# Kernel tuning notes

Measured on AMD Instinct MI355X. Metric: run time of the kernel, lower is better.

The kernel has to match this reference:

```python
import jax, jax.numpy as jnp
import numpy as np


def _lstm_gates(z, c):
    # Keras LSTMCell gate order: i, f, c(candidate), o
    i, f, g, o = jnp.split(z, 4, axis=-1)
    c_new = jax.nn.sigmoid(f) * c + jax.nn.sigmoid(i) * jnp.tanh(g)
    h_new = jax.nn.sigmoid(o) * jnp.tanh(c_new)
    return h_new, c_new


def setup_inputs() -> dict:
    key = jax.random.key(0)
    ks = jax.random.split(key, 12)
    BS, T, F, Z, H = 8192, 20, 80, 32, 256
    s = 0.05
    return {
        "x": jax.random.normal(ks[0], (BS, T, F), jnp.float32),
        "z1": jax.random.normal(ks[1], (BS, Z), jnp.float32),
        "z2": jax.random.normal(ks[2], (BS, Z), jnp.float32),
        "eps": jax.random.normal(ks[3], (BS, T, F), jnp.float32),
        "W1": jax.random.normal(ks[4], (2 * Z, 4 * H), jnp.float32) * s,
        "U1": jax.random.normal(ks[5], (H, 4 * H), jnp.float32) * s,
        "b1": jnp.zeros((4 * H,), jnp.float32),
        "W2": jax.random.normal(ks[6], (H, 4 * H), jnp.float32) * s,
        "U2": jax.random.normal(ks[7], (H, 4 * H), jnp.float32) * s,
        "b2": jnp.zeros((4 * H,), jnp.float32),
        "Wmu": jax.random.normal(ks[8], (H, F), jnp.float32) * s,
        "bmu": jnp.zeros((F,), jnp.float32),
        "Wlv": jax.random.normal(ks[9], (H, F), jnp.float32) * s,
        "blv": jnp.zeros((F,), jnp.float32),
    }


def reference(x, z1, z2, eps, W1, U1, b1, W2, U2, b2, Wmu, bmu, Wlv, blv):
    bs, T = x.shape[0], x.shape[1]
    H = U1.shape[0]
    # z1,z2 are tiled across time -> per-step RNN input is constant, so the
    # input projection of layer 1 can be hoisted out of the scan.
    z_cat = jnp.concatenate([z1, z2], axis=-1)          # [bs, 2Z]
    xw1 = z_cat @ W1 + b1                                # [bs, 4H] constant per step

    def step(carry, _):
        h1, c1, h2, c2 = carry
        h1n, c1n = _lstm_gates(xw1 + h1 @ U1, c1)
        h2n, c2n = _lstm_gates(h1n @ W2 + b2 + h2 @ U2, c2)
        return (h1n, c1n, h2n, c2n), h2n

    zero = jnp.zeros((bs, H), x.dtype)
    _, hs = jax.lax.scan(step, (zero, zero, zero, zero), None, length=T)
    output = jnp.transpose(hs, (1, 0, 2))                # [bs, T, H]

    x_mu = output @ Wmu + bmu                            # [bs, T, F]
    x_logvar = output @ Wlv + blv                        # [bs, T, F]
    # NOTE: original code calls reparameterize(x_logvar_t, x_mu_t) with
    # swapped arguments -> sample = eps * exp(0.5 * x_mu) + x_logvar
    x_sample = eps * jnp.exp(0.5 * x_mu) + x_logvar
    return output, x_mu, x_logvar, x_sample
```

## Files before the change

### kernel.cpp

```cpp
#include <hip/hip_runtime.h>
#include <cstdint>
#include <cstddef>

typedef __bf16 bf16_t;
typedef __attribute__((ext_vector_type(8))) __bf16 bf16x8;
typedef __attribute__((ext_vector_type(4))) __bf16 bf16x4;
typedef __attribute__((ext_vector_type(4))) float f32x4;

#define TSTEPS 20
#define HDIM 256
#define GDIM 1024

static __device__ __forceinline__ f32x4 mfma_(bf16x8 a, bf16x8 b, f32x4 c) {
    return __builtin_amdgcn_mfma_f32_16x16x32_bf16(a, b, c, 0, 0, 0);
}
static __device__ __forceinline__ float sig_(float x) {
    return __builtin_amdgcn_rcpf(1.0f + __expf(-x));
}
static __device__ __forceinline__ float tanh_(float x) {
    return 2.0f * __builtin_amdgcn_rcpf(1.0f + __expf(-2.0f * x)) - 1.0f;
}

__global__ void pack_b_kernel(const float* __restrict__ srcA, int ldA,
                              const float* __restrict__ srcB, int ldB,
                              int split, int ntiles, int ktiles,
                              bf16_t* __restrict__ dst)
{
    int tid = blockIdx.x * blockDim.x + threadIdx.x;
    int total = ntiles * ktiles * 64;
    if (tid >= total) return;
    int lane = tid & 63;
    int tile = tid >> 6;
    int kt = tile % ktiles;
    int nt = tile / ktiles;
    int c  = (nt << 4) + (lane & 15);
    int k0 = (kt << 5) + ((lane >> 4) << 3);
    bf16x8 v;
    #pragma unroll
    for (int e = 0; e < 8; ++e) {
        int k = k0 + e;
        float x;
        if (c < split) x = srcA[(size_t)k * ldA + c];
        else           x = srcB[(size_t)k * ldB + (c - split)];
        v[e] = (bf16_t)x;
    }
    *reinterpret_cast<bf16x8*>(&dst[(size_t)tid * 8]) = v;
}

__global__ __launch_bounds__(256, 1)
void lstm_scan_kernel(const float* __restrict__ z1, const float* __restrict__ z2,
                      const float* __restrict__ W1, const float* __restrict__ b1,
                      const float* __restrict__ b2,
                      const bf16_t* __restrict__ U1p, const bf16_t* __restrict__ B2p,
                      float* __restrict__ out)
{
    __shared__ alignas(16) bf16_t xw1T[GDIM * 32];
    __shared__ alignas(16) bf16_t h1buf[2 * 32 * HDIM];
    __shared__ alignas(16) bf16_t h2buf[2 * 32 * HDIM];
    __shared__ alignas(16) float  zT[64 * 32];

    const int tid  = threadIdx.x;
    const int lane = tid & 63;
    const int wv   = tid >> 6;
    const int l15  = lane & 15;
    const int lq   = lane >> 4;
    const int w4   = wv << 2;
    const int b0   = blockIdx.x << 5;

    for (int i = tid; i < 2048; i += 256) {
        int r = i >> 6, k = i & 63;
        float v = (k < 32) ? z1[(size_t)(b0 + r) * 32 + k]
                           : z2[(size_t)(b0 + r) * 32 + (k - 32)];
        zT[k * 32 + r] = v;
    }
    for (int i = tid; i < 8192; i += 256) {
        h1buf[i] = (bf16_t)0.0f;
        h2buf[i] = (bf16_t)0.0f;
    }
    __syncthreads();

    for (int cc = 0; cc < 4; ++cc) {
        const int c = tid + (cc << 8);
        float acc[32];
        #pragma unroll
        for (int r = 0; r < 32; ++r) acc[r] = 0.0f;
        for (int k = 0; k < 64; ++k) {
            float wk = W1[k * GDIM + c];
            const f32x4* zp = reinterpret_cast<const f32x4*>(&zT[k * 32]);
            #pragma unroll
            for (int rq = 0; rq < 8; ++rq) {
                f32x4 z4 = zp[rq];
                #pragma unroll
                for (int j = 0; j < 4; ++j) acc[rq * 4 + j] += z4[j] * wk;
            }
        }
        const float bb = b1[c];
        const int sw = (c & 7) << 2;
        #pragma unroll
        for (int r = 0; r < 32; ++r)
            xw1T[((c << 5) + r) ^ sw] = (bf16_t)(acc[r] + bb);
    }

    float b2r[4][4];
    #pragma unroll
    for (int g = 0; g < 4; ++g)
        #pragma unroll
        for (int ht = 0; ht < 4; ++ht)
            b2r[g][ht] = b2[(((g << 4) + w4 + ht) << 4) + l15];

    f32x4 c1[2][4], c2[2][4];
    #pragma unroll
    for (int mt = 0; mt < 2; ++mt)
        #pragma unroll
        for (int ht = 0; ht < 4; ++ht) {
            c1[mt][ht] = (f32x4){0.f, 0.f, 0.f, 0.f};
            c2[mt][ht] = (f32x4){0.f, 0.f, 0.f, 0.f};
        }

    __syncthreads();

    bf16x8 af[2][16];
    const size_t outbase = (size_t)b0 * (TSTEPS * HDIM);

    for (int t = 0; t < TSTEPS; ++t) {
        const int cur = (t & 1) << 13;
        const int nxt = 8192 - cur;

        #pragma unroll
        for (int mt = 0; mt < 2; ++mt)
            #pragma unroll
            for (int kt = 0; kt < 8; ++kt) {
                int row = (mt << 4) + l15;
                int k0  = (kt << 5) + (lq << 3);
                int off = (((row << 8) + k0)) ^ ((row & 7) << 3);
                af[mt][kt] = *reinterpret_cast<const bf16x8*>(&h1buf[cur + off]);
            }

        #pragma unroll
        for (int ht = 0; ht < 4; ++ht) {
            f32x4 ag[2][4];
            #pragma unroll
            for (int g = 0; g < 4; ++g) {
                const int ntg  = (g << 4) + w4 + ht;
                const int colb = (ntg << 4) + l15;
                {
                    const int sw = (colb & 7) << 2;
                    int idx0 = ((colb << 5) + (lq << 2)) ^ sw;
                    int idx1 = ((colb << 5) + 16 + (lq << 2)) ^ sw;
                    bf16x4 v0 = *reinterpret_cast<const bf16x4*>(&xw1T[idx0]);
                    bf16x4 v1 = *reinterpret_cast<const bf16x4*>(&xw1T[idx1]);
                    f32x4 a0, a1;
                    #pragma unroll
                    for (int j = 0; j < 4; ++j) { a0[j] = (float)v0[j]; a1[j] = (float)v1[j]; }
                    ag[0][g] = a0; ag[1][g] = a1;
                }
                const bf16x8* bp = reinterpret_cast<const bf16x8*>(U1p) + ((ntg << 3) << 6) + lane;
                #pragma unroll
                for (int kt = 0; kt < 8; ++kt) {
                    bf16x8 bfr = bp[kt << 6];
                    ag[0][g] = mfma_(af[0][kt], bfr, ag[0][g]);
                    ag[1][g] = mfma_(af[1][kt], bfr, ag[1][g]);
                }
            }
            const int col = ((w4 + ht) << 4) + l15;
            #pragma unroll
            for (int mt = 0; mt < 2; ++mt)
                #pragma unroll
                for (int j = 0; j < 4; ++j) {
                    float iv = sig_(ag[mt][0][j]);
                    float fv = sig_(ag[mt][1][j]);
                    float gv = tanh_(ag[mt][2][j]);
                    float ov = sig_(ag[mt][3][j]);
                    float cn = fv * c1[mt][ht][j] + iv * gv;
                    c1[mt][ht][j] = cn;
                    float hn = ov * tanh_(cn);
                    int row = (mt << 4) + (lq << 2) + j;
                    h1buf[nxt + (((row << 8) + col) ^ ((row & 7) << 3))] = (bf16_t)hn;
                }
        }
        __syncthreads();

        #pragma unroll
        for (int mt = 0; mt < 2; ++mt)
            #pragma unroll
            for (int kt = 0; kt < 8; ++kt) {
                int row = (mt << 4) + l15;
                int k0  = (kt << 5) + (lq << 3);
                int off = (((row << 8) + k0)) ^ ((row & 7) << 3);
                af[mt][kt]     = *reinterpret_cast<const bf16x8*>(&h1buf[nxt + off]);
                af[mt][8 + kt] = *reinterpret_cast<const bf16x8*>(&h2buf[cur + off]);
            }

        #pragma unroll
        for (int ht = 0; ht < 4; ++ht) {
            f32x4 ag[2][4];
            #pragma unroll
            for (int g = 0; g < 4; ++g) {
                const int ntg = (g << 4) + w4 + ht;
                const float bb = b2r[g][ht];
                ag[0][g] = (f32x4){bb, bb, bb, bb};
                ag[1][g] = (f32x4){bb, bb, bb, bb};
                const bf16x8* bp0 = reinterpret_cast<const bf16x8*>(B2p) + ((ntg << 3) << 6) + lane;
                const bf16x8* bp1 = reinterpret_cast<const bf16x8*>(B2p) + (((64 + ntg) << 3) << 6) + lane;
                #pragma unroll
                for (int kt = 0; kt < 8; ++kt) {
                    bf16x8 bfr = bp0[kt << 6];
                    ag[0][g] = mfma_(af[0][kt], bfr, ag[0][g]);
                    ag[1][g] = mfma_(af[1][kt], bfr, ag[1][g]);
                }
                #pragma unroll
                for (int kt = 0; kt < 8; ++kt) {
                    bf16x8 bfr = bp1[kt << 6];
                    ag[0][g] = mfma_(af[0][8 + kt], bfr, ag[0][g]);
                    ag[1][g] = mfma_(af[1][8 + kt], bfr, ag[1][g]);
                }
            }
            const int col = ((w4 + ht) << 4) + l15;
            #pragma unroll
            for (int mt = 0; mt < 2; ++mt)
                #pragma unroll
                for (int j = 0; j < 4; ++j) {
                    float iv = sig_(ag[mt][0][j]);
                    float fv = sig_(ag[mt][1][j]);
                    float gv = tanh_(ag[mt][2][j]);
                    float ov = sig_(ag[mt][3][j]);
                    float cn = fv * c2[mt][ht][j] + iv * gv;
                    c2[mt][ht][j] = cn;
                    float hn = ov * tanh_(cn);
                    int row = (mt << 4) + (lq << 2) + j;
                    h2buf[nxt + (((row << 8) + col) ^ ((row & 7) << 3))] = (bf16_t)hn;
                    out[outbase + (size_t)row * (TSTEPS * HDIM) + t * HDIM + col] = hn;
                }
        }
        __syncthreads();
    }
}

__global__ __launch_bounds__(256, 1)
void proj_kernel(const float* __restrict__ outp, const float* __restrict__ eps,
                 const float* __restrict__ bmu, const float* __restrict__ blv,
                 const bf16_t* __restrict__ Wpp,
                 float* __restrict__ xmu, float* __restrict__ xlv, float* __restrict__ xsm)
{
    const int tid = threadIdx.x, lane = tid & 63, wv = tid >> 6;
    const int l15 = lane & 15, lq = lane >> 4;
    const size_t r0 = (size_t)blockIdx.x * 128 + (size_t)wv * 32;

    bf16x8 af[2][8];
    #pragma unroll
    for (int mt = 0; mt < 2; ++mt)
        #pragma unroll
        for (int kt = 0; kt < 8; ++kt) {
            const float* p = &outp[(r0 + (mt << 4) + l15) * 256 + (kt << 5) + (lq << 3)];
            f32x4 x0 = *reinterpret_cast<const f32x4*>(p);
            f32x4 x1 = *reinterpret_cast<const f32x4*>(p + 4);
            bf16x8 a;
            #pragma unroll
            for (int j = 0; j < 4; ++j) { a[j] = (bf16_t)x0[j]; a[4 + j] = (bf16_t)x1[j]; }
            af[mt][kt] = a;
        }

    f32x4 acc[2][10];
    #pragma unroll
    for (int mt = 0; mt < 2; ++mt)
        #pragma unroll
        for (int nt = 0; nt < 10; ++nt) acc[mt][nt] = (f32x4){0.f, 0.f, 0.f, 0.f};

    #pragma unroll
    for (int nt = 0; nt < 10; ++nt) {
        const bf16x8* bp = reinterpret_cast<const bf16x8*>(Wpp) + ((nt << 3) << 6) + lane;
        #pragma unroll
        for (int kt = 0; kt < 8; ++kt) {
            bf16x8 b = bp[kt << 6];
            acc[0][nt] = mfma_(af[0][kt], b, acc[0][nt]);
            acc[1][nt] = mfma_(af[1][kt], b, acc[1][nt]);
        }
    }

    #pragma unroll
    for (int mt = 0; mt < 2; ++mt)
        #pragma unroll
        for (int nt = 0; nt < 5; ++nt) {
            const int col = (nt << 4) + l15;
            const float bm = bmu[col], bl = blv[col];
            #pragma unroll
            for (int j = 0; j < 4; ++j) {
                size_t row = r0 + (mt << 4) + (lq << 2) + j;
                float mu = acc[mt][nt][j] + bm;
                float lv = acc[mt][5 + nt][j] + bl;
                size_t o = row * 80 + col;
                float sm = eps[o] * __expf(0.5f * mu) + lv;
                xmu[o] = mu; xlv[o] = lv; xsm[o] = sm;
            }
        }
}

extern "C" void kernel_launch(void* const* d_in, const int* in_sizes, int n_in,
                              void* d_out, int out_size, void* d_ws, size_t ws_size,
                              hipStream_t stream) {
    const float* z1  = (const float*)d_in[1];
    const float* z2  = (const float*)d_in[2];
    const float* eps = (const float*)d_in[3];
    const float* W1  = (const float*)d_in[4];
    const float* U1  = (const float*)d_in[5];
    const float* b1  = (const float*)d_in[6];
    const float* W2  = (const float*)d_in[7];
    const float* U2  = (const float*)d_in[8];
    const float* b2  = (const float*)d_in[9];
    const float* Wmu = (const float*)d_in[10];
    const float* bmu = (const float*)d_in[11];
    const float* Wlv = (const float*)d_in[12];
    const float* blv = (const float*)d_in[13];

    float* out0 = (float*)d_out;
    const size_t N_OUT = (size_t)8192 * 20 * 256;
    const size_t N_F   = (size_t)8192 * 20 * 80;
    float* xmu = out0 + N_OUT;
    float* xlv = xmu + N_F;
    float* xsm = xlv + N_F;

    bf16_t* U1p = (bf16_t*)d_ws;
    bf16_t* B2p = U1p + 262144;
    bf16_t* Wpp = U1p + 786432;

    pack_b_kernel<<<128, 256, 0, stream>>>(U1, 1024, U1, 1024, 1 << 30, 64, 8, U1p);
    pack_b_kernel<<<128, 256, 0, stream>>>(W2, 1024, W2, 1024, 1 << 30, 64, 8, B2p);
    pack_b_kernel<<<128, 256, 0, stream>>>(U2, 1024, U2, 1024, 1 << 30, 64, 8, B2p + 262144);
    pack_b_kernel<<<20, 256, 0, stream>>>(Wmu, 80, Wlv, 80, 80, 10, 8, Wpp);

    lstm_scan_kernel<<<256, 256, 0, stream>>>(z1, z2, W1, b1, b2, U1p, B2p, out0);
    proj_kernel<<<1280, 256, 0, stream>>>(out0, eps, bmu, blv, Wpp, xmu, xlv, xsm);
}
```

Measured before the change: 2.741 ms.

## Recompute layer-1 input projection via MFMA, double scan waves, restage proj via LDS

The scan kernel now runs 512 threads per block, with each wave owning two hidden tiles instead of four. It drops the scalar fp32 precompute of the z@W1 projection held in LDS and recomputes that projection with MFMA every step from packed bf16 W1, which frees LDS and registers. The projection kernel stages 64 rows through a swizzled LDS buffer before its MFMA, and outputs are written with nontemporal stores. This trades extra per-step MFMA work and a W1 pack for better occupancy and latency hiding in the serial scan.

```diff
diff --git a/kernel.cpp b/kernel.cpp
--- a/kernel.cpp
+++ b/kernel.cpp
@@ -8,8 +8,6 @@
 typedef __attribute__((ext_vector_type(4))) float f32x4;
 
 #define TSTEPS 20
-#define HDIM 256
-#define GDIM 1024
 
 static __device__ __forceinline__ f32x4 mfma_(bf16x8 a, bf16x8 b, f32x4 c) {
     return __builtin_amdgcn_mfma_f32_16x16x32_bf16(a, b, c, 0, 0, 0);
@@ -19,6 +17,9 @@
 }
 static __device__ __forceinline__ float tanh_(float x) {
     return 2.0f * __builtin_amdgcn_rcpf(1.0f + __expf(-2.0f * x)) - 1.0f;
+}
+static __device__ __forceinline__ int swz(int row, int k) {
+    return ((row << 8) + k) ^ ((row & 7) << 3);
 }
 
 __global__ void pack_b_kernel(const float* __restrict__ srcA, int ldA,
@@ -47,252 +48,272 @@
     *reinterpret_cast<bf16x8*>(&dst[(size_t)tid * 8]) = v;
 }
 
-__global__ __launch_bounds__(256, 1)
+__global__ __launch_bounds__(512, 2)
 void lstm_scan_kernel(const float* __restrict__ z1, const float* __restrict__ z2,
-                      const float* __restrict__ W1, const float* __restrict__ b1,
-                      const float* __restrict__ b2,
-                      const bf16_t* __restrict__ U1p, const bf16_t* __restrict__ B2p,
+                      const float* __restrict__ b1, const float* __restrict__ b2,
+                      const bf16x8* __restrict__ W1f, const bf16x8* __restrict__ U1f,
+                      const bf16x8* __restrict__ B2f,
                       float* __restrict__ out)
 {
-    __shared__ alignas(16) bf16_t xw1T[GDIM * 32];
-    __shared__ alignas(16) bf16_t h1buf[2 * 32 * HDIM];
-    __shared__ alignas(16) bf16_t h2buf[2 * 32 * HDIM];
-    __shared__ alignas(16) float  zT[64 * 32];
+    __shared__ alignas(16) bf16_t h1buf[2 * 32 * 256];
+    __shared__ alignas(16) bf16_t h2buf[2 * 32 * 256];
+    __shared__ alignas(16) bf16_t zc[32 * 64];
 
     const int tid  = threadIdx.x;
     const int lane = tid & 63;
     const int wv   = tid >> 6;
     const int l15  = lane & 15;
     const int lq   = lane >> 4;
-    const int w4   = wv << 2;
     const int b0   = blockIdx.x << 5;
 
-    for (int i = tid; i < 2048; i += 256) {
+    {
+        bf16x8 z8;
+        #pragma unroll
+        for (int j = 0; j < 8; ++j) z8[j] = (bf16_t)0.0f;
+        bf16x8* h1v = reinterpret_cast<bf16x8*>(h1buf);
+        bf16x8* h2v = reinterpret_cast<bf16x8*>(h2buf);
+        for (int i = tid; i < 2048; i += 512) { h1v[i] = z8; h2v[i] = z8; }
+    }
+    for (int i = tid; i < 2048; i += 512) {
         int r = i >> 6, k = i & 63;
         float v = (k < 32) ? z1[(size_t)(b0 + r) * 32 + k]
                            : z2[(size_t)(b0 + r) * 32 + (k - 32)];
-        zT[k * 32 + r] = v;
-    }
-    for (int i = tid; i < 8192; i += 256) {
-        h1buf[i] = (bf16_t)0.0f;
-        h2buf[i] = (bf16_t)0.0f;
+        zc[i] = (bf16_t)v;
     }
     __syncthreads();
 
-    for (int cc = 0; cc < 4; ++cc) {
-        const int c = tid + (cc << 8);
-        float acc[32];
-        #pragma unroll
-        for (int r = 0; r < 32; ++r) acc[r] = 0.0f;
-        for (int k = 0; k < 64; ++k) {
-            float wk = W1[k * GDIM + c];
-            const f32x4* zp = reinterpret_cast<const f32x4*>(&zT[k * 32]);
-            #pragma unroll
-            for (int rq = 0; rq < 8; ++rq) {
-                f32x4 z4 = zp[rq];
-                #pragma unroll
-                for (int j = 0; j < 4; ++j) acc[rq * 4 + j] += z4[j] * wk;
-            }
-        }
-        const float bb = b1[c];
-        const int sw = (c & 7) << 2;
-        #pragma unroll
-        for (int r = 0; r < 32; ++r)
-            xw1T[((c << 5) + r) ^ sw] = (bf16_t)(acc[r] + bb);
-    }
-
-    float b2r[4][4];
-    #pragma unroll
-    for (int g = 0; g < 4; ++g)
-        #pragma unroll
-        for (int ht = 0; ht < 4; ++ht)
-            b2r[g][ht] = b2[(((g << 4) + w4 + ht) << 4) + l15];
-
-    f32x4 c1[2][4], c2[2][4];
+    bf16x8 zf[2][2];
     #pragma unroll
     for (int mt = 0; mt < 2; ++mt)
         #pragma unroll
-        for (int ht = 0; ht < 4; ++ht) {
+        for (int kt = 0; kt < 2; ++kt)
+            zf[mt][kt] = *reinterpret_cast<const bf16x8*>(
+                &zc[((mt << 4) + l15) * 64 + (kt << 5) + (lq << 3)]);
+
+    float b1r[2][4], b2r[2][4];
+    #pragma unroll
+    for (int ht = 0; ht < 2; ++ht)
+        #pragma unroll
+        for (int g = 0; g < 4; ++g) {
+            const int ntg = (g << 4) + (wv << 1) + ht;
+            b1r[ht][g] = b1[(ntg << 4) + l15];
+            b2r[ht][g] = b2[(ntg << 4) + l15];
+        }
+
+    f32x4 c1[2][2], c2[2][2];
+    #pragma unroll
+    for (int mt = 0; mt < 2; ++mt)
+        #pragma unroll
+        for (int ht = 0; ht < 2; ++ht) {
             c1[mt][ht] = (f32x4){0.f, 0.f, 0.f, 0.f};
             c2[mt][ht] = (f32x4){0.f, 0.f, 0.f, 0.f};
         }
 
-    __syncthreads();
-
-    bf16x8 af[2][16];
-    const size_t outbase = (size_t)b0 * (TSTEPS * HDIM);
+    const size_t outbase = (size_t)b0 * (TSTEPS * 256);
 
     for (int t = 0; t < TSTEPS; ++t) {
         const int cur = (t & 1) << 13;
         const int nxt = 8192 - cur;
 
-        #pragma unroll
-        for (int mt = 0; mt < 2; ++mt)
-            #pragma unroll
-            for (int kt = 0; kt < 8; ++kt) {
-                int row = (mt << 4) + l15;
-                int k0  = (kt << 5) + (lq << 3);
-                int off = (((row << 8) + k0)) ^ ((row & 7) << 3);
-                af[mt][kt] = *reinterpret_cast<const bf16x8*>(&h1buf[cur + off]);
+        f32x4 ag[2][2][4];
+        #pragma unroll
+        for (int ht = 0; ht < 2; ++ht)
+            #pragma unroll
+            for (int g = 0; g < 4; ++g) {
+                const float b = b1r[ht][g];
+                ag[ht][0][g] = (f32x4){b, b, b, b};
+                ag[ht][1][g] = (f32x4){b, b, b, b};
             }
 
-        #pragma unroll
-        for (int ht = 0; ht < 4; ++ht) {
-            f32x4 ag[2][4];
-            #pragma unroll
-            for (int g = 0; g < 4; ++g) {
-                const int ntg  = (g << 4) + w4 + ht;
-                const int colb = (ntg << 4) + l15;
-                {
-                    const int sw = (colb & 7) << 2;
-                    int idx0 = ((colb << 5) + (lq << 2)) ^ sw;
-                    int idx1 = ((colb << 5) + 16 + (lq << 2)) ^ sw;
-                    bf16x4 v0 = *reinterpret_cast<const bf16x4*>(&xw1T[idx0]);
-                    bf16x4 v1 = *reinterpret_cast<const bf16x4*>(&xw1T[idx1]);
-                    f32x4 a0, a1;
+        {
+            bf16x8 af[2][8];
+            #pragma unroll
+            for (int mt = 0; mt < 2; ++mt)
+                #pragma unroll
+                for (int kt = 0; kt < 8; ++kt) {
+                    int row = (mt << 4) + l15;
+                    af[mt][kt] = *reinterpret_cast<const bf16x8*>(
+                        &h1buf[cur + swz(row, (kt << 5) + (lq << 3))]);
+                }
+            #pragma unroll
+            for (int ht = 0; ht < 2; ++ht)
+                #pragma unroll
+                for (int g = 0; g < 4; ++g) {
+                    const int ntg = (g << 4) + (wv << 1) + ht;
+                    const bf16x8* wz = W1f + ((ntg << 1) << 6) + lane;
                     #pragma unroll
-                    for (int j = 0; j < 4; ++j) { a0[j] = (float)v0[j]; a1[j] = (float)v1[j]; }
-                    ag[0][g] = a0; ag[1][g] = a1;
-                }
-                const bf16x8* bp = reinterpret_cast<const bf16x8*>(U1p) + ((ntg << 3) << 6) + lane;
-                #pragma unroll
-                for (int kt = 0; kt < 8; ++kt) {
-                    bf16x8 bfr = bp[kt << 6];
-                    ag[0][g] = mfma_(af[0][kt], bfr, ag[0][g]);
-                    ag[1][g] = mfma_(af[1][kt], bfr, ag[1][g]);
-                }
-            }
-            const int col = ((w4 + ht) << 4) + l15;
+                    for (int kt = 0; kt < 2; ++kt) {
+                        bf16x8 w = wz[kt << 6];
+                        ag[ht][0][g] = mfma_(zf[0][kt], w, ag[ht][0][g]);
+                        ag[ht][1][g] = mfma_(zf[1][kt], w, ag[ht][1][g]);
+                    }
+                    const bf16x8* wu = U1f + ((ntg << 3) << 6) + lane;
+                    #pragma unroll
+                    for (int kt = 0; kt < 8; ++kt) {
+                        bf16x8 w = wu[kt << 6];
+                        ag[ht][0][g] = mfma_(af[0][kt], w, ag[ht][0][g]);
+                        ag[ht][1][g] = mfma_(af[1][kt], w, ag[ht][1][g]);
+                    }
+                }
+        }
+        #pragma unroll
+        for (int ht = 0; ht < 2; ++ht) {
+            const int colb = (((wv << 1) + ht) << 4) + l15;
             #pragma unroll
             for (int mt = 0; mt < 2; ++mt)
                 #pragma unroll
                 for (int j = 0; j < 4; ++j) {
-                    float iv = sig_(ag[mt][0][j]);
-                    float fv = sig_(ag[mt][1][j]);
-                    float gv = tanh_(ag[mt][2][j]);
-                    float ov = sig_(ag[mt][3][j]);
+                    float iv = sig_(ag[ht][mt][0][j]);
+                    float fv = sig_(ag[ht][mt][1][j]);
+                    float gv = tanh_(ag[ht][mt][2][j]);
+                    float ov = sig_(ag[ht][mt][3][j]);
                     float cn = fv * c1[mt][ht][j] + iv * gv;
                     c1[mt][ht][j] = cn;
                     float hn = ov * tanh_(cn);
                     int row = (mt << 4) + (lq << 2) + j;
-                    h1buf[nxt + (((row << 8) + col) ^ ((row & 7) << 3))] = (bf16_t)hn;
+                    h1buf[nxt + swz(row, colb)] = (bf16_t)hn;
                 }
         }
         __syncthreads();
 
         #pragma unroll
-        for (int mt = 0; mt < 2; ++mt)
-            #pragma unroll
-            for (int kt = 0; kt < 8; ++kt) {
-                int row = (mt << 4) + l15;
-                int k0  = (kt << 5) + (lq << 3);
-                int off = (((row << 8) + k0)) ^ ((row & 7) << 3);
-                af[mt][kt]     = *reinterpret_cast<const bf16x8*>(&h1buf[nxt + off]);
-                af[mt][8 + kt] = *reinterpret_cast<const bf16x8*>(&h2buf[cur + off]);
+        for (int ht = 0; ht < 2; ++ht)
+            #pragma unroll
+            for (int g = 0; g < 4; ++g) {
+                const float b = b2r[ht][g];
+                ag[ht][0][g] = (f32x4){b, b, b, b};
+                ag[ht][1][g] = (f32x4){b, b, b, b};
             }
-
-        #pragma unroll
-        for (int ht = 0; ht < 4; ++ht) {
-            f32x4 ag[2][4];
-            #pragma unroll
-            for (int g = 0; g < 4; ++g) {
-                const int ntg = (g << 4) + w4 + ht;
-                const float bb = b2r[g][ht];
-                ag[0][g] = (f32x4){bb, bb, bb, bb};
-                ag[1][g] = (f32x4){bb, bb, bb, bb};
-                const bf16x8* bp0 = reinterpret_cast<const bf16x8*>(B2p) + ((ntg << 3) << 6) + lane;
-                const bf16x8* bp1 = reinterpret_cast<const bf16x8*>(B2p) + (((64 + ntg) << 3) << 6) + lane;
+        {
+            bf16x8 af[2][8];
+            #pragma unroll
+            for (int mt = 0; mt < 2; ++mt)
                 #pragma unroll
                 for (int kt = 0; kt < 8; ++kt) {
-                    bf16x8 bfr = bp0[kt << 6];
-                    ag[0][g] = mfma_(af[0][kt], bfr, ag[0][g]);
-                    ag[1][g] = mfma_(af[1][kt], bfr, ag[1][g]);
-                }
+                    int row = (mt << 4) + l15;
+                    af[mt][kt] = *reinterpret_cast<const bf16x8*>(
+                        &h1buf[nxt + swz(row, (kt << 5) + (lq << 3))]);
+                }
+            #pragma unroll
+            for (int ht = 0; ht < 2; ++ht)
+                #pragma unroll
+                for (int g = 0; g < 4; ++g) {
+                    const int ntg = (g << 4) + (wv << 1) + ht;
+                    const bf16x8* w2 = B2f + ((ntg << 3) << 6) + lane;
+                    #pragma unroll
+                    for (int kt = 0; kt < 8; ++kt) {
+                        bf16x8 w = w2[kt << 6];
+                        ag[ht][0][g] = mfma_(af[0][kt], w, ag[ht][0][g]);
+                        ag[ht][1][g] = mfma_(af[1][kt], w, ag[ht][1][g]);
+                    }
+                }
+            #pragma unroll
+            for (int mt = 0; mt < 2; ++mt)
                 #pragma unroll
                 for (int kt = 0; kt < 8; ++kt) {
-                    bf16x8 bfr = bp1[kt << 6];
-                    ag[0][g] = mfma_(af[0][8 + kt], bfr, ag[0][g]);
-                    ag[1][g] = mfma_(af[1][8 + kt], bfr, ag[1][g]);
-                }
-            }
-            const int col = ((w4 + ht) << 4) + l15;
+                    int row = (mt << 4) + l15;
+                    af[mt][kt] = *reinterpret_cast<const bf16x8*>(
+                        &h2buf[cur + swz(row, (kt << 5) + (lq << 3))]);
+                }
+            #pragma unroll
+            for (int ht = 0; ht < 2; ++ht)
+                #pragma unroll
+                for (int g = 0; g < 4; ++g) {
+                    const int ntg = (g << 4) + (wv << 1) + ht;
+                    const bf16x8* u2 = B2f + (((64 + ntg) << 3) << 6) + lane;
+                    #pragma unroll
+                    for (int kt = 0; kt < 8; ++kt) {
+                        bf16x8 w = u2[kt << 6];
+                        ag[ht][0][g] = mfma_(af[0][kt], w, ag[ht][0][g]);
+                        ag[ht][1][g] = mfma_(af[1][kt], w, ag[ht][1][g]);
+                    }
+                }
+        }
+        #pragma unroll
+        for (int ht = 0; ht < 2; ++ht) {
+            const int colb = (((wv << 1) + ht) << 4) + l15;
             #pragma unroll
             for (int mt = 0; mt < 2; ++mt)
                 #pragma unroll
                 for (int j = 0; j < 4; ++j) {
-                    float iv = sig_(ag[mt][0][j]);
-                    float fv = sig_(ag[mt][1][j]);
-                    float gv = tanh_(ag[mt][2][j]);
-                    float ov = sig_(ag[mt][3][j]);
+                    float iv = sig_(ag[ht][mt][0][j]);
+                    float fv = sig_(ag[ht][mt][1][j]);
+                    float gv = tanh_(ag[ht][mt][2][j]);
+                    float ov = sig_(ag[ht][mt][3][j]);
                     float cn = fv * c2[mt][ht][j] + iv * gv;
                     c2[mt][ht][j] = cn;
                     float hn = ov * tanh_(cn);
                     int row = (mt << 4) + (lq << 2) + j;
-                    h2buf[nxt + (((row << 8) + col) ^ ((row & 7) << 3))] = (bf16_t)hn;
-                    out[outbase + (size_t)row * (TSTEPS * HDIM) + t * HDIM + col] = hn;
+                    h2buf[nxt + swz(row, colb)] = (bf16_t)hn;
+                    __builtin_nontemporal_store(
+                        hn, &out[outbase + (size_t)row * (TSTEPS * 256) + t * 256 + colb]);
                 }
         }
         __syncthreads();
     }
 }
 
-__global__ __launch_bounds__(256, 1)
+__global__ __launch_bounds__(256)
 void proj_kernel(const float* __restrict__ outp, const float* __restrict__ eps,
                  const float* __restrict__ bmu, const float* __restrict__ blv,
-                 const bf16_t* __restrict__ Wpp,
+                 const bf16x8* __restrict__ Wpf,
                  float* __restrict__ xmu, float* __restrict__ xlv, float* __restrict__ xsm)
 {
+    __shared__ alignas(16) bf16_t sbuf[64 * 256];
+
     const int tid = threadIdx.x, lane = tid & 63, wv = tid >> 6;
     const int l15 = lane & 15, lq = lane >> 4;
-    const size_t r0 = (size_t)blockIdx.x * 128 + (size_t)wv * 32;
-
-    bf16x8 af[2][8];
-    #pragma unroll
-    for (int mt = 0; mt < 2; ++mt)
-        #pragma unroll
-        for (int kt = 0; kt < 8; ++kt) {
-            const float* p = &outp[(r0 + (mt << 4) + l15) * 256 + (kt << 5) + (lq << 3)];
-            f32x4 x0 = *reinterpret_cast<const f32x4*>(p);
-            f32x4 x1 = *reinterpret_cast<const f32x4*>(p + 4);
-            bf16x8 a;
-            #pragma unroll
-            for (int j = 0; j < 4; ++j) { a[j] = (bf16_t)x0[j]; a[4 + j] = (bf16_t)x1[j]; }
-            af[mt][kt] = a;
-        }
-
-    f32x4 acc[2][10];
-    #pragma unroll
-    for (int mt = 0; mt < 2; ++mt)
-        #pragma unroll
-        for (int nt = 0; nt < 10; ++nt) acc[mt][nt] = (f32x4){0.f, 0.f, 0.f, 0.f};
+    const size_t r0 = (size_t)blockIdx.x * 64;
+
+    const float* src = &outp[r0 * 256];
+    #pragma unroll
+    for (int it = 0; it < 16; ++it) {
+        int e = (it << 10) + (tid << 2);
+        int row = e >> 8, col = e & 255;
+        f32x4 v = *reinterpret_cast<const f32x4*>(&src[e]);
+        bf16x4 b;
+        #pragma unroll
+        for (int j = 0; j < 4; ++j) b[j] = (bf16_t)v[j];
+        *reinterpret_cast<bf16x4*>(&sbuf[swz(row, col)]) = b;
+    }
+    __syncthreads();
+
+    bf16x8 af[8];
+    #pragma unroll
+    for (int kt = 0; kt < 8; ++kt) {
+        int row = (wv << 4) + l15;
+        af[kt] = *reinterpret_cast<const bf16x8*>(
+            &sbuf[swz(row, (kt << 5) + (lq << 3))]);
+    }
+
+    f32x4 acc[10];
+    #pragma unroll
+    for (int nt = 0; nt < 10; ++nt) acc[nt] = (f32x4){0.f, 0.f, 0.f, 0.f};
 
     #pragma unroll
     for (int nt = 0; nt < 10; ++nt) {
-        const bf16x8* bp = reinterpret_cast<const bf16x8*>(Wpp) + ((nt << 3) << 6) + lane;
-        #pragma unroll
-        for (int kt = 0; kt < 8; ++kt) {
-            bf16x8 b = bp[kt << 6];
-            acc[0][nt] = mfma_(af[0][kt], b, acc[0][nt]);
-            acc[1][nt] = mfma_(af[1][kt], b, acc[1][nt]);
-        }
-    }
-
-    #pragma unroll
-    for (int mt = 0; mt < 2; ++mt)
-        #pragma unroll
-        for (int nt = 0; nt < 5; ++nt) {
-            const int col = (nt << 4) + l15;
-            const float bm = bmu[col], bl = blv[col];
-            #pragma unroll
-            for (int j = 0; j < 4; ++j) {
-                size_t row = r0 + (mt << 4) + (lq << 2) + j;
-                float mu = acc[mt][nt][j] + bm;
-                float lv = acc[mt][5 + nt][j] + bl;
-                size_t o = row * 80 + col;
-                float sm = eps[o] * __expf(0.5f * mu) + lv;
-                xmu[o] = mu; xlv[o] = lv; xsm[o] = sm;
-            }
-        }
+        const bf16x8* bp = Wpf + ((nt << 3) << 6) + lane;
+        #pragma unroll
+        for (int kt = 0; kt < 8; ++kt)
+            acc[nt] = mfma_(af[kt], bp[kt << 6], acc[nt]);
+    }
+
+    #pragma unroll
+    for (int nt = 0; nt < 5; ++nt) {
+        const int col = (nt << 4) + l15;
+        const float bm = bmu[col], bl = blv[col];
+        #pragma unroll
+        for (int j = 0; j < 4; ++j) {
+            size_t row = r0 + (wv << 4) + (lq << 2) + j;
+            float mu = acc[nt][j] + bm;
+            float lv = acc[5 + nt][j] + bl;
+            size_t o = row * 80 + col;
+            float sm = eps[o] * __expf(0.5f * mu) + lv;
+            __builtin_nontemporal_store(mu, &xmu[o]);
+            __builtin_nontemporal_store(lv, &xlv[o]);
+            __builtin_nontemporal_store(sm, &xsm[o]);
+        }
+    }
 }
 
 extern "C" void kernel_launch(void* const* d_in, const int* in_sizes, int n_in,
@@ -319,15 +340,20 @@
     float* xlv = xmu + N_F;
     float* xsm = xlv + N_F;
 
-    bf16_t* U1p = (bf16_t*)d_ws;
+    bf16_t* W1p = (bf16_t*)d_ws;
+    bf16_t* U1p = W1p + 65536;
     bf16_t* B2p = U1p + 262144;
-    bf16_t* Wpp = U1p + 786432;
-
+    bf16_t* Wpp = B2p + 524288;
+
+    pack_b_kernel<<<32, 256, 0, stream>>>(W1, 1024, W1, 1024, 1 << 30, 64, 2, W1p);
     pack_b_kernel<<<128, 256, 0, stream>>>(U1, 1024, U1, 1024, 1 << 30, 64, 8, U1p);
     pack_b_kernel<<<128, 256, 0, stream>>>(W2, 1024, W2, 1024, 1 << 30, 64, 8, B2p);
     pack_b_kernel<<<128, 256, 0, stream>>>(U2, 1024, U2, 1024, 1 << 30, 64, 8, B2p + 262144);
     pack_b_kernel<<<20, 256, 0, stream>>>(Wmu, 80, Wlv, 80, 80, 10, 8, Wpp);
 
-    lstm_scan_kernel<<<256, 256, 0, stream>>>(z1, z2, W1, b1, b2, U1p, B2p, out0);
-    proj_kernel<<<1280, 256, 0, stream>>>(out0, eps, bmu, blv, Wpp, xmu, xlv, xsm);
-}
+    lstm_scan_kernel<<<256, 512, 0, stream>>>(z1, z2, b1, b2,
+                                              (const bf16x8*)W1p, (const bf16x8*)U1p,
+                                              (const bf16x8*)B2p, out0);
+    proj_kernel<<<2560, 256, 0, stream>>>(out0, eps, bmu, blv,
+                                          (const bf16x8*)Wpp, xmu, xlv, xsm);
+}
```

Result: slower. 2.800 ms (+2.2%).
